# Kernel tuning notes

Hardware: AMD Instinct MI355X
Metric: run time of the kernel (lower is better)

The kernel has to match this reference:

```python
import jax, jax.numpy as jnp
import numpy as np

U = 200000   # num_users
I = 100000   # num_items
N = U + I    # total homogeneous nodes
E = 1000000  # bipartite interaction edges
D = 64       # embed_dim (== audio feature dim)
A = 20000    # num_artists
AL = 50000   # num_albums
ATTR = 8     # edge_mlp_input_dim
H = 32       # edge_mlp_hidden_dim
L = 3        # num_layers
AUDIO_SCALE = 1.0
META_SCALE = 1.0
EPS = 1e-12


def l2norm(x):
    # F.normalize(p=2, dim=-1, eps=1e-12)
    n = jnp.sqrt(jnp.sum(x * x, axis=-1, keepdims=True))
    return x / jnp.maximum(n, EPS)


def setup_inputs() -> dict:
    key = jax.random.key(0)
    ks = jax.random.split(key, 12)
    return {
        "edge_src": jax.random.randint(ks[0], (E,), 0, U, dtype=jnp.int32),
        "edge_dst": jax.random.randint(ks[1], (E,), 0, I, dtype=jnp.int32),
        "edge_attr": jax.random.normal(ks[2], (E, ATTR), dtype=jnp.float32),
        "user_w": jax.random.normal(ks[3], (U, D), dtype=jnp.float32) * 0.1,
        "artist_w": jax.random.normal(ks[4], (A, D), dtype=jnp.float32) * 0.1,
        "album_w": jax.random.normal(ks[5], (AL, D), dtype=jnp.float32) * 0.1,
        "item_audio": jax.random.normal(ks[6], (I, D), dtype=jnp.float32),
        "artist_ids": jax.random.randint(ks[7], (I,), 0, A, dtype=jnp.int32),
        "album_ids": jax.random.randint(ks[8], (I,), 0, AL, dtype=jnp.int32),
        "Wp": jax.random.normal(ks[9], (2 * D, D), dtype=jnp.float32) * (1.0 / np.sqrt(2 * D)),
        "bp": jnp.zeros((D,), dtype=jnp.float32),
        "W1": jax.random.normal(ks[10], (ATTR, H), dtype=jnp.float32) * (1.0 / np.sqrt(ATTR)),
        "b1": jnp.zeros((H,), dtype=jnp.float32),
        "W2": jax.random.normal(ks[11], (H, 1), dtype=jnp.float32) * (1.0 / np.sqrt(H)),
        "b2": jnp.zeros((1,), dtype=jnp.float32),
    }


def reference(edge_src, edge_dst, edge_attr, user_w, artist_w, album_w,
              item_audio, artist_ids, album_ids, Wp, bp, W1, b1, W2, b2):
    # --- edge-weight MLP: Linear -> ReLU -> Linear -> Sigmoid, clamp ---
    h = jax.nn.relu(edge_attr @ W1 + b1)          # [E, H]
    w = jax.nn.sigmoid(h @ W2 + b2)[:, 0]          # [E]
    w = jnp.maximum(w, 1e-6)

    # --- homogeneous graph: fwd, bwd, remaining self loops (fill=1.0) ---
    dst = edge_dst.astype(jnp.int32) + U
    loop = jnp.arange(N, dtype=jnp.int32)
    row = jnp.concatenate([edge_src, dst, loop])   # source nodes
    col = jnp.concatenate([dst, edge_src, loop])   # target nodes
    ew = jnp.concatenate([w, w, jnp.ones((N,), w.dtype)])

    # --- gcn_norm (LGConv normalize=True, add_self_loops=False inside) ---
    deg = jax.ops.segment_sum(ew, col, num_segments=N)
    dis = jnp.where(deg > 0, jax.lax.rsqrt(deg), 0.0)
    norm = dis[row] * ew * dis[col]                # [2E + N]

    # --- initial node features ---
    user = l2norm(user_w)                          # [U, D]
    meta = (artist_w[artist_ids] + album_w[album_ids]) * META_SCALE
    item_in = jnp.concatenate([item_audio * AUDIO_SCALE, meta], axis=-1)  # [I, 2D]
    item = l2norm(item_in @ Wp + bp)               # [I, D]
    x = jnp.concatenate([user, item], axis=0)      # [N, D]

    # --- L rounds of LGConv propagation, layer-sum readout ---
    acc = x
    for _ in range(L):
        x = jax.ops.segment_sum(norm[:, None] * x[row], col, num_segments=N)
        acc = acc + x
    x = l2norm(acc / (L + 1))
    return x[:U], x[U:]
```

## Files before the change

kernel.cpp:

```cpp
#include <hip/hip_runtime.h>
#include <hip/hip_bf16.h>

#define U_CNT 200000
#define I_CNT 100000
#define N_CNT 300000
#define E_CNT 1000000
#define ATTR_D 8
#define H_DIM 32
#define NB_SCAN ((N_CNT + 255) / 256)
#define IB 128
#define NB_I ((I_CNT + IB - 1) / IB)
#define NB_META (I_CNT / 16)
#define XP 130

#define BSHIFT 10
#define NBUCK 293
#define BCAP 12288
#define EPB 2048
#define NB_BIN1 ((E_CNT + EPB - 1) / EPB)


typedef unsigned short ubf;

__device__ __forceinline__ float b2f(ubf b) {
    return __uint_as_float((unsigned)b << 16);
}
__device__ __forceinline__ ubf f2b(float v) {
    unsigned u = __float_as_uint(v);
    u += 0x7fffu + ((u >> 16) & 1u);
    return (ubf)(u >> 16);
}
__device__ __forceinline__ unsigned pk2(float lo, float hi) {
    return (unsigned)f2b(lo) | ((unsigned)f2b(hi) << 16);
}
__device__ __forceinline__ float4 b4f(ushort4 u) {
    return make_float4(b2f(u.x), b2f(u.y), b2f(u.z), b2f(u.w));
}
__device__ __forceinline__ uint2 packE(int key, int partner, unsigned wb) {
    return make_uint2((unsigned)key | (((unsigned)partner & 0x1FFFu) << 19),
                     ((unsigned)partner >> 13) | (wb << 16));
}

__global__ void k_meta(const float* __restrict__ art, const float* __restrict__ alb,
                       const int* __restrict__ aid, const int* __restrict__ alid,
                       ubf* __restrict__ metabuf, int* __restrict__ gcur) {
    int t = threadIdx.x;
    if (blockIdx.x == 0) {
        for (int i = t; i < NBUCK; i += 256) gcur[i] = i * BCAP;
    }
    int lane = t & 63;
    int g = lane >> 4;
    int q = lane & 15;
    int wv = (blockIdx.x * 256 + t) >> 6;
    int it = wv * 4 + g;
    if (it >= I_CNT) return;
    int a_ = aid[it], al_ = alid[it];
    float4 va = *(const float4*)&art[(size_t)a_ * 64 + q * 4];
    float4 vb = *(const float4*)&alb[(size_t)al_ * 64 + q * 4];
    ushort4 o = make_ushort4(f2b(va.x + vb.x), f2b(va.y + vb.y),
                             f2b(va.z + vb.z), f2b(va.w + vb.w));
    *(ushort4*)&metabuf[(size_t)it * 64 + q * 4] = o;
}

__global__ void __launch_bounds__(512)
k_bin1(const int* __restrict__ src, const int* __restrict__ dst,
       const float* __restrict__ attr,
       const float* __restrict__ W1, const float* __restrict__ b1,
       const float* __restrict__ W2, const float* __restrict__ b2,
       uint2* __restrict__ ebuf, int* __restrict__ gcur) {
    __shared__ float sW1[ATTR_D * H_DIM];
    __shared__ float sb1[H_DIM];
    __shared__ float sW2[H_DIM];
    __shared__ float sb2;
    __shared__ int hist[NBUCK];
    __shared__ int basem[NBUCK];
    int t = threadIdx.x;
    if (t < 256) sW1[t] = W1[t];
    if (t < H_DIM) { sb1[t] = b1[t]; sW2[t] = W2[t]; }
    if (t == 0) sb2 = b2[0];
    for (int i = t; i < NBUCK; i += 512) hist[i] = 0;
    __syncthreads();
    int ebase = blockIdx.x * EPB;
    int sarr[4], darr[4];
    unsigned warr[4];
    #pragma unroll
    for (int k = 0; k < 4; ++k) {
        int e = ebase + k * 512 + t;
        sarr[k] = -1;
        if (e < E_CNT) {
            const float4* a4 = (const float4*)attr + (size_t)e * 2;
            float4 r0 = a4[0];
            float4 r1 = a4[1];
            float a[8] = {r0.x, r0.y, r0.z, r0.w, r1.x, r1.y, r1.z, r1.w};
            float z = sb2;
            #pragma unroll
            for (int h = 0; h < H_DIM; ++h) {
                float acc = sb1[h];
                #pragma unroll
                for (int kk = 0; kk < 8; ++kk) acc = fmaf(a[kk], sW1[kk * H_DIM + h], acc);
                acc = fmaxf(acc, 0.0f);
                z = fmaf(acc, sW2[h], z);
            }
            float w = 1.0f / (1.0f + __expf(-z));
            w = fmaxf(w, 1e-6f);
            int s = src[e], d = U_CNT + dst[e];
            sarr[k] = s; darr[k] = d; warr[k] = (unsigned)f2b(w);
            atomicAdd(&hist[s >> BSHIFT], 1);
            atomicAdd(&hist[d >> BSHIFT], 1);
        }
    }
    __syncthreads();
    for (int i = t; i < NBUCK; i += 512) {
        int h = hist[i];
        basem[i] = (h > 0) ? atomicAdd(&gcur[i], h) : 0;
    }
    __syncthreads();
    for (int i = t; i < NBUCK; i += 512) hist[i] = 0;
    __syncthreads();
    #pragma unroll
    for (int k = 0; k < 4; ++k) {
        if (sarr[k] >= 0) {
            int s = sarr[k], d = darr[k];
            unsigned wb = warr[k];
            int bs = s >> BSHIFT;
            int r = atomicAdd(&hist[bs], 1);
            ebuf[(size_t)basem[bs] + r] = packE(s, d, wb);
            int bd = d >> BSHIFT;
            r = atomicAdd(&hist[bd], 1);
            ebuf[(size_t)basem[bd] + r] = packE(d, s, wb);
        }
    }
}

__global__ void __launch_bounds__(1024)
k_bin2(const uint2* __restrict__ ebuf, const int* __restrict__ gcur,
       int* __restrict__ offs, int2* __restrict__ csr,
       float* __restrict__ dis) {
    __shared__ int ldsCnt[NBUCK];
    __shared__ int ldsH[1024];
    __shared__ int ldsC[1024];
    __shared__ int ldsT[1024];
    __shared__ float ldsW[1024];
    __shared__ int sMeta[2];
    int t = threadIdx.x;
    int b = blockIdx.x;
    if (t < NBUCK) ldsCnt[t] = gcur[t] - t * BCAP;
    ldsH[t] = 0;
    ldsC[t] = 0;
    ldsW[t] = 0.0f;
    __syncthreads();
    if (t == 0) {
        int base = 0;
        for (int i = 0; i < b; ++i) base += ldsCnt[i];
        sMeta[0] = base;
        sMeta[1] = ldsCnt[b];
    }
    __syncthreads();
    int csr_base = sMeta[0], mycount = sMeta[1];
    size_t eb = (size_t)b * BCAP;
    int first = b << BSHIFT;
    for (int i = t; i < mycount; i += 1024) {
        uint2 en = ebuf[eb + i];
        atomicAdd(&ldsH[(en.x & 0x7FFFFu) - first], 1);
    }
    __syncthreads();
    int v0 = ldsH[t];
    ldsT[t] = v0;
    __syncthreads();
    #pragma unroll
    for (int off = 1; off < 1024; off <<= 1) {
        int x = (t >= off) ? ldsT[t - off] : 0;
        __syncthreads();
        ldsT[t] += x;
        __syncthreads();
    }
    int excl = ldsT[t] - v0;
    ldsH[t] = excl;
    __syncthreads();
    int ncnt = min(1024, N_CNT - first);
    if (t < ncnt) offs[first + t] = csr_base + ldsH[t];
    if (b == NBUCK - 1 && t == 0) offs[N_CNT] = 2 * E_CNT;
    for (int i = t; i < mycount; i += 1024) {
        uint2 en = ebuf[eb + i];
        int key = (int)(en.x & 0x7FFFFu);
        int partner = (int)((en.x >> 19) | ((en.y & 0xFFFFu) << 13));
        unsigned wb = en.y >> 16;
        int li = key - first;
        int r = atomicAdd(&ldsC[li], 1);
        csr[csr_base + ldsH[li] + r] = make_int2(partner, (int)(wb << 16));
        atomicAdd(&ldsW[li], b2f((ubf)wb));
    }
    __syncthreads();
    if (t < ncnt) dis[first + t] = rsqrtf(1.0f + ldsW[t]);
}

__global__ void k_users(const float* __restrict__ user_w, const float* __restrict__ dis,
                        ubf* __restrict__ y0, float* __restrict__ acc, int use_acc) {
    int lane = threadIdx.x & 63;
    int wv = (blockIdx.x * blockDim.x + threadIdx.x) >> 6;
    int nw = (gridDim.x * blockDim.x) >> 6;
    for (int r = wv; r < U_CNT; r += nw) {
        int idx = r * 64 + lane;
        float v = user_w[idx];
        float ss = v * v;
        #pragma unroll
        for (int m = 32; m >= 1; m >>= 1) ss += __shfl_xor(ss, m, 64);
        float inv = dis[r] / fmaxf(sqrtf(ss), 1e-12f);
        float o = v * inv;
        y0[idx] = f2b(o);
        if (use_acc) acc[idx] = o;
    }
}

__global__ void __launch_bounds__(256)
k_items(const float* __restrict__ audio, const ubf* __restrict__ metabuf,
        const float* __restrict__ Wp, const float* __restrict__ bp,
        const float* __restrict__ dis,
        ubf* __restrict__ yitem, float* __restrict__ accitem, int use_acc) {
    __shared__ __align__(16) ubf sXT[128 * XP];
    __shared__ __align__(16) ubf sW[128 * 64];
    int t = threadIdx.x;
    int base = blockIdx.x * IB;
    {
        const float4* wg = (const float4*)Wp;
        #pragma unroll
        for (int r = 0; r < 8; ++r) {
            int idx = r * 256 + t;
            float4 v = wg[idx];
            ushort4 o = make_ushort4(f2b(v.x), f2b(v.y), f2b(v.z), f2b(v.w));
            *(ushort4*)&sW[idx * 4] = o;
        }
    }
    {
        const float4* g = (const float4*)audio + (size_t)base * 16;
        #pragma unroll
        for (int r = 0; r < 8; ++r) {
            int idx = r * 256 + t;
            int i = idx >> 4, fq = idx & 15;
            float4 v = make_float4(0.f, 0.f, 0.f, 0.f);
            if (base + i < I_CNT) v = g[idx];
            sXT[(4 * fq + 0) * XP + i] = f2b(v.x);
            sXT[(4 * fq + 1) * XP + i] = f2b(v.y);
            sXT[(4 * fq + 2) * XP + i] = f2b(v.z);
            sXT[(4 * fq + 3) * XP + i] = f2b(v.w);
        }
    }
    {
        const uint4* m4 = (const uint4*)(metabuf + (size_t)base * 64);
        #pragma unroll
        for (int r = 0; r < 4; ++r) {
            int idx = r * 256 + t;
            int i = idx >> 3, c = idx & 7;
            uint4 m = make_uint4(0u, 0u, 0u, 0u);
            if (base + i < I_CNT) m = m4[idx];
            ubf* dp = &sXT[(64 + 8 * c) * XP + i];
            dp[0 * XP] = (ubf)(m.x & 0xffffu); dp[1 * XP] = (ubf)(m.x >> 16);
            dp[2 * XP] = (ubf)(m.y & 0xffffu); dp[3 * XP] = (ubf)(m.y >> 16);
            dp[4 * XP] = (ubf)(m.z & 0xffffu); dp[5 * XP] = (ubf)(m.z >> 16);
            dp[6 * XP] = (ubf)(m.w & 0xffffu); dp[7 * XP] = (ubf)(m.w >> 16);
        }
    }
    __syncthreads();
    int og = t & 7;
    int igr = t >> 3;
    float c[4][8];
    {
        float bv[8];
        #pragma unroll
        for (int j = 0; j < 8; ++j) bv[j] = bp[8 * og + j];
        #pragma unroll
        for (int i = 0; i < 4; ++i)
            #pragma unroll
            for (int j = 0; j < 8; ++j) c[i][j] = bv[j];
    }
    const ubf* xcol = &sXT[4 * igr];
    const ubf* wrow = &sW[8 * og];
    #pragma unroll 2
    for (int k = 0; k < 128; ++k) {
        ushort4 xu = *(const ushort4*)&xcol[k * XP];
        uint4 wu = *(const uint4*)&wrow[k * 64];
        float x[4] = {b2f(xu.x), b2f(xu.y), b2f(xu.z), b2f(xu.w)};
        float w[8];
        w[0] = __uint_as_float(wu.x << 16); w[1] = __uint_as_float(wu.x & 0xffff0000u);
        w[2] = __uint_as_float(wu.y << 16); w[3] = __uint_as_float(wu.y & 0xffff0000u);
        w[4] = __uint_as_float(wu.z << 16); w[5] = __uint_as_float(wu.z & 0xffff0000u);
        w[6] = __uint_as_float(wu.w << 16); w[7] = __uint_as_float(wu.w & 0xffff0000u);
        #pragma unroll
        for (int i = 0; i < 4; ++i)
            #pragma unroll
            for (int j = 0; j < 8; ++j) c[i][j] = fmaf(x[i], w[j], c[i][j]);
    }
    #pragma unroll
    for (int i = 0; i < 4; ++i) {
        float ss = 0.f;
        #pragma unroll
        for (int j = 0; j < 8; ++j) ss += c[i][j] * c[i][j];
        ss += __shfl_xor(ss, 1, 64);
        ss += __shfl_xor(ss, 2, 64);
        ss += __shfl_xor(ss, 4, 64);
        int it = base + 4 * igr + i;
        if (it < I_CNT) {
            float q = dis[U_CNT + it] / fmaxf(sqrtf(ss), 1e-12f);
            uint4 o;
            o.x = pk2(c[i][0] * q, c[i][1] * q);
            o.y = pk2(c[i][2] * q, c[i][3] * q);
            o.z = pk2(c[i][4] * q, c[i][5] * q);
            o.w = pk2(c[i][6] * q, c[i][7] * q);
            *(uint4*)&yitem[(size_t)it * 64 + 8 * og] = o;
            if (use_acc) {
                float4* ap = (float4*)&accitem[(size_t)it * 64 + 8 * og];
                ap[0] = make_float4(c[i][0] * q, c[i][1] * q, c[i][2] * q, c[i][3] * q);
                ap[1] = make_float4(c[i][4] * q, c[i][5] * q, c[i][6] * q, c[i][7] * q);
            }
        }
    }
}

__device__ __forceinline__ void prop_gather(const int* offs, const int2* csr,
                                            const ubf* yin, int c, int s4,
                                            float4& a0, float4& a1,
                                            float4& a2, float4& a3) {
    int e = offs[c], end = offs[c + 1];
    for (; e + 7 < end; e += 8) {
        int2 e0 = csr[e], e1 = csr[e + 1], e2 = csr[e + 2], e3 = csr[e + 3];
        int2 e4 = csr[e + 4], e5 = csr[e + 5], e6 = csr[e + 6], e7 = csr[e + 7];
        ushort4 g0 = *(const ushort4*)&yin[(size_t)e0.x * 64 + s4];
        ushort4 g1 = *(const ushort4*)&yin[(size_t)e1.x * 64 + s4];
        ushort4 g2 = *(const ushort4*)&yin[(size_t)e2.x * 64 + s4];
        ushort4 g3 = *(const ushort4*)&yin[(size_t)e3.x * 64 + s4];
        ushort4 g4 = *(const ushort4*)&yin[(size_t)e4.x * 64 + s4];
        ushort4 g5 = *(const ushort4*)&yin[(size_t)e5.x * 64 + s4];
        ushort4 g6 = *(const ushort4*)&yin[(size_t)e6.x * 64 + s4];
        ushort4 g7 = *(const ushort4*)&yin[(size_t)e7.x * 64 + s4];
        float w0 = __int_as_float(e0.y), w1 = __int_as_float(e1.y);
        float w2 = __int_as_float(e2.y), w3 = __int_as_float(e3.y);
        float w4 = __int_as_float(e4.y), w5 = __int_as_float(e5.y);
        float w6 = __int_as_float(e6.y), w7 = __int_as_float(e7.y);
        float4 f0 = b4f(g0), f1 = b4f(g1), f2 = b4f(g2), f3 = b4f(g3);
        float4 f4 = b4f(g4), f5 = b4f(g5), f6 = b4f(g6), f7 = b4f(g7);
        a0.x = fmaf(w0, f0.x, a0.x); a0.y = fmaf(w0, f0.y, a0.y);
        a0.z = fmaf(w0, f0.z, a0.z); a0.w = fmaf(w0, f0.w, a0.w);
        a1.x = fmaf(w1, f1.x, a1.x); a1.y = fmaf(w1, f1.y, a1.y);
        a1.z = fmaf(w1, f1.z, a1.z); a1.w = fmaf(w1, f1.w, a1.w);
        a2.x = fmaf(w2, f2.x, a2.x); a2.y = fmaf(w2, f2.y, a2.y);
        a2.z = fmaf(w2, f2.z, a2.z); a2.w = fmaf(w2, f2.w, a2.w);
        a3.x = fmaf(w3, f3.x, a3.x); a3.y = fmaf(w3, f3.y, a3.y);
        a3.z = fmaf(w3, f3.z, a3.z); a3.w = fmaf(w3, f3.w, a3.w);
        a0.x = fmaf(w4, f4.x, a0.x); a0.y = fmaf(w4, f4.y, a0.y);
        a0.z = fmaf(w4, f4.z, a0.z); a0.w = fmaf(w4, f4.w, a0.w);
        a1.x = fmaf(w5, f5.x, a1.x); a1.y = fmaf(w5, f5.y, a1.y);
        a1.z = fmaf(w5, f5.z, a1.z); a1.w = fmaf(w5, f5.w, a1.w);
        a2.x = fmaf(w6, f6.x, a2.x); a2.y = fmaf(w6, f6.y, a2.y);
        a2.z = fmaf(w6, f6.z, a2.z); a2.w = fmaf(w6, f6.w, a2.w);
        a3.x = fmaf(w7, f7.x, a3.x); a3.y = fmaf(w7, f7.y, a3.y);
        a3.z = fmaf(w7, f7.z, a3.z); a3.w = fmaf(w7, f7.w, a3.w);
    }
    for (; e + 3 < end; e += 4) {
        int2 e0 = csr[e], e1 = csr[e + 1], e2 = csr[e + 2], e3 = csr[e + 3];
        ushort4 g0 = *(const ushort4*)&yin[(size_t)e0.x * 64 + s4];
        ushort4 g1 = *(const ushort4*)&yin[(size_t)e1.x * 64 + s4];
        ushort4 g2 = *(const ushort4*)&yin[(size_t)e2.x * 64 + s4];
        ushort4 g3 = *(const ushort4*)&yin[(size_t)e3.x * 64 + s4];
        float w0 = __int_as_float(e0.y), w1 = __int_as_float(e1.y);
        float w2 = __int_as_float(e2.y), w3 = __int_as_float(e3.y);
        float4 f0 = b4f(g0), f1 = b4f(g1), f2 = b4f(g2), f3 = b4f(g3);
        a0.x = fmaf(w0, f0.x, a0.x); a0.y = fmaf(w0, f0.y, a0.y);
        a0.z = fmaf(w0, f0.z, a0.z); a0.w = fmaf(w0, f0.w, a0.w);
        a1.x = fmaf(w1, f1.x, a1.x); a1.y = fmaf(w1, f1.y, a1.y);
        a1.z = fmaf(w1, f1.z, a1.z); a1.w = fmaf(w1, f1.w, a1.w);
        a2.x = fmaf(w2, f2.x, a2.x); a2.y = fmaf(w2, f2.y, a2.y);
        a2.z = fmaf(w2, f2.z, a2.z); a2.w = fmaf(w2, f2.w, a2.w);
        a3.x = fmaf(w3, f3.x, a3.x); a3.y = fmaf(w3, f3.y, a3.y);
        a3.z = fmaf(w3, f3.z, a3.z); a3.w = fmaf(w3, f3.w, a3.w);
    }
    for (; e < end; ++e) {
        int2 ee = csr[e];
        ushort4 gg = *(const ushort4*)&yin[(size_t)ee.x * 64 + s4];
        float ww = __int_as_float(ee.y);
        float4 ff = b4f(gg);
        a0.x = fmaf(ww, ff.x, a0.x); a0.y = fmaf(ww, ff.y, a0.y);
        a0.z = fmaf(ww, ff.z, a0.z); a0.w = fmaf(ww, ff.w, a0.w);
    }
}

__global__ void k_prop(const int* __restrict__ offs, const int2* __restrict__ csr,
                       const float* __restrict__ dis,
                       const ubf* __restrict__ yin, ubf* __restrict__ yout,
                       float* __restrict__ acc, int use_acc) {
    int lane = threadIdx.x & 63;
    int g = lane >> 4;
    int s4 = (lane & 15) * 4;
    int wv = (blockIdx.x * 256 + threadIdx.x) >> 6;
    int c = wv * 4 + g;
    if (c >= N_CNT) return;
    float dc = dis[c];
    float4 a0 = make_float4(0.f, 0.f, 0.f, 0.f);
    float4 a1 = a0, a2 = a0, a3 = a0;
    prop_gather(offs, csr, yin, c, s4, a0, a1, a2, a3);
    size_t idx = (size_t)c * 64 + s4;
    float4 self = b4f(*(const ushort4*)&yin[idx]);
    float dc2 = dc * dc;
    float4 r;
    r.x = dc2 * (((a0.x + a1.x) + (a2.x + a3.x)) + self.x);
    r.y = dc2 * (((a0.y + a1.y) + (a2.y + a3.y)) + self.y);
    r.z = dc2 * (((a0.z + a1.z) + (a2.z + a3.z)) + self.z);
    r.w = dc2 * (((a0.w + a1.w) + (a2.w + a3.w)) + self.w);
    *(ushort4*)&yout[idx] = make_ushort4(f2b(r.x), f2b(r.y), f2b(r.z), f2b(r.w));
    if (use_acc) {
        float4* ap = (float4*)&acc[idx];
        float4 av = *ap;
        av.x += r.x; av.y += r.y; av.z += r.z; av.w += r.w;
        *ap = av;
    }
}

__global__ void k_prop_fin(const int* __restrict__ offs, const int2* __restrict__ csr,
                           const float* __restrict__ dis,
                           const ubf* __restrict__ y0, const ubf* __restrict__ y1,
                           const ubf* __restrict__ yin, float* __restrict__ out) {
    int lane = threadIdx.x & 63;
    int g = lane >> 4;
    int s4 = (lane & 15) * 4;
    int wv = (blockIdx.x * 256 + threadIdx.x) >> 6;
    int c = wv * 4 + g;
    if (c >= N_CNT) return;
    float dc = dis[c];
    float4 a0 = make_float4(0.f, 0.f, 0.f, 0.f);
    float4 a1 = a0, a2 = a0, a3 = a0;
    prop_gather(offs, csr, yin, c, s4, a0, a1, a2, a3);
    size_t idx = (size_t)c * 64 + s4;
    float4 self = b4f(*(const ushort4*)&yin[idx]);
    float dc2 = dc * dc;
    float4 r;
    r.x = dc2 * (((a0.x + a1.x) + (a2.x + a3.x)) + self.x);
    r.y = dc2 * (((a0.y + a1.y) + (a2.y + a3.y)) + self.y);
    r.z = dc2 * (((a0.z + a1.z) + (a2.z + a3.z)) + self.z);
    r.w = dc2 * (((a0.w + a1.w) + (a2.w + a3.w)) + self.w);
    float4 v0 = b4f(*(const ushort4*)&y0[idx]);
    float4 v1 = b4f(*(const ushort4*)&y1[idx]);
    float4 v;
    v.x = (v0.x + v1.x) + (self.x + r.x);
    v.y = (v0.y + v1.y) + (self.y + r.y);
    v.z = (v0.z + v1.z) + (self.z + r.z);
    v.w = (v0.w + v1.w) + (self.w + r.w);
    float ss = v.x * v.x + v.y * v.y + v.z * v.z + v.w * v.w;
    ss += __shfl_xor(ss, 1, 64);
    ss += __shfl_xor(ss, 2, 64);
    ss += __shfl_xor(ss, 4, 64);
    ss += __shfl_xor(ss, 8, 64);
    float inv = 1.0f / fmaxf(sqrtf(ss), 1e-12f);
    *(float4*)&out[idx] = make_float4(v.x * inv, v.y * inv, v.z * inv, v.w * inv);
}

__global__ void k_final_acc(const float* __restrict__ acc, float* __restrict__ out) {
    int lane = threadIdx.x & 63;
    int c = (blockIdx.x * 256 + threadIdx.x) >> 6;
    if (c >= N_CNT) return;
    int idx = c * 64 + lane;
    float v = acc[idx];
    float ss = v * v;
    #pragma unroll
    for (int m = 32; m >= 1; m >>= 1) ss += __shfl_xor(ss, m, 64);
    out[idx] = v / fmaxf(sqrtf(ss), 1e-12f);
}

extern "C" void kernel_launch(void* const* d_in, const int* in_sizes, int n_in,
                              void* d_out, int out_size, void* d_ws, size_t ws_size,
                              hipStream_t stream) {
    const int*   edge_src   = (const int*)  d_in[0];
    const int*   edge_dst   = (const int*)  d_in[1];
    const float* edge_attr  = (const float*)d_in[2];
    const float* user_w     = (const float*)d_in[3];
    const float* artist_w   = (const float*)d_in[4];
    const float* album_w    = (const float*)d_in[5];
    const float* item_audio = (const float*)d_in[6];
    const int*   artist_ids = (const int*)  d_in[7];
    const int*   album_ids  = (const int*)  d_in[8];
    const float* Wp         = (const float*)d_in[9];
    const float* bp         = (const float*)d_in[10];
    const float* W1         = (const float*)d_in[11];
    const float* b1         = (const float*)d_in[12];
    const float* W2         = (const float*)d_in[13];
    const float* b2         = (const float*)d_in[14];

    char* p = (char*)d_ws;
    auto carve = [&](size_t bytes) -> void* {
        void* q = (void*)p;
        p += (bytes + 255) & ~(size_t)255;
        return q;
    };
    float* dis    = (float*)carve((size_t)N_CNT * 4);
    int*   offs   = (int*)  carve((size_t)(N_CNT + 1) * 4);
    int*   gcur   = (int*)  carve((size_t)NBUCK * 4);
    int2*  csr    = (int2*) carve((size_t)2 * E_CNT * 8);
    ubf*   metabuf= (ubf*)  carve((size_t)I_CNT * 64 * 2);
    const size_t YB = (size_t)N_CNT * 64 * 2;
    const size_t EBUF = (size_t)NBUCK * BCAP * 8;
    size_t used = (size_t)(p - (char*)d_ws);
    int no_acc = (ws_size >= used + 3 * YB + (size_t)4096) ? 1 : 0;
    ubf *y0, *y1, *y2;
    uint2* ebuf;
    float* acc = nullptr;
    if (no_acc) {
        y0 = (ubf*)carve(YB);
        y1 = (ubf*)carve(YB);
        y2 = (ubf*)carve(YB);
        ebuf = (uint2*)y2;
    } else {
        y0 = (ubf*)carve(YB);
        y1 = (ubf*)carve(YB);
        y2 = y0;
        acc = (float*)d_out;
        ebuf = (uint2*)carve(EBUF);
    }
    (void)in_sizes; (void)n_in; (void)out_size;

    k_meta <<<NB_META, 256, 0, stream>>>(artist_w, album_w, artist_ids,
                                         album_ids, metabuf, gcur);
    k_bin1 <<<NB_BIN1, 512, 0, stream>>>(edge_src, edge_dst, edge_attr,
                                         W1, b1, W2, b2, ebuf, gcur);
    k_bin2 <<<NBUCK, 1024, 0, stream>>>(ebuf, gcur, offs, csr, dis);
    k_users<<<1024, 256, 0, stream>>>(user_w, dis, y0, acc, no_acc ? 0 : 1);
    k_items<<<NB_I, 256, 0, stream>>>(item_audio, metabuf, Wp, bp, dis,
                                      y0 + (size_t)U_CNT * 64,
                                      no_acc ? nullptr : acc + (size_t)U_CNT * 64,
                                      no_acc ? 0 : 1);
    const int PROP_BLKS = N_CNT / 16;
    if (no_acc) {
        k_prop<<<PROP_BLKS, 256, 0, stream>>>(offs, csr, dis, y0, y1, nullptr, 0);
        k_prop<<<PROP_BLKS, 256, 0, stream>>>(offs, csr, dis, y1, y2, nullptr, 0);
        k_prop_fin<<<PROP_BLKS, 256, 0, stream>>>(offs, csr, dis, y0, y1, y2,
                                                  (float*)d_out);
    } else {
        k_prop<<<PROP_BLKS, 256, 0, stream>>>(offs, csr, dis, y0, y1, acc, 1);
        k_prop<<<PROP_BLKS, 256, 0, stream>>>(offs, csr, dis, y1, y0, acc, 1);
        k_prop<<<PROP_BLKS, 256, 0, stream>>>(offs, csr, dis, y0, y1, acc, 1);
        k_final_acc<<<N_CNT / 4, 256, 0, stream>>>(acc, (float*)d_out);
    }
}
```

Measured before the change: 513.2 us.

## Use 8 lanes per node in propagation, fuse meta into binning, wave-scan in bin2

The propagation kernels now give each node 8 lanes that each load 16 bytes (8 bf16 values), in place of 16 lanes loading 8 bytes. This halves the CSR index loads per node and widens each gather, with two accumulator sets for ILP. The meta-embedding kernel is folded into extra blocks of the binning kernel, and gcur is cleared with a memset, which removes one launch. The block scan in bin2 is replaced by a wavefront shuffle scan plus a 16-entry serial scan, which cuts the barrier count. The trade-off is lower lane parallelism per node, which may hurt latency hiding for high-degree nodes.

```diff
diff --git a/kernel.cpp b/kernel.cpp
--- a/kernel.cpp
+++ b/kernel.cpp
@@ -7,10 +7,8 @@
 #define E_CNT 1000000
 #define ATTR_D 8
 #define H_DIM 32
-#define NB_SCAN ((N_CNT + 255) / 256)
 #define IB 128
 #define NB_I ((I_CNT + IB - 1) / IB)
-#define NB_META (I_CNT / 16)
 #define XP 130
 
 #define BSHIFT 10
@@ -18,6 +16,7 @@
 #define BCAP 12288
 #define EPB 2048
 #define NB_BIN1 ((E_CNT + EPB - 1) / EPB)
+#define NB_META5 (I_CNT / 32)
 
 
 typedef unsigned short ubf;
@@ -33,33 +32,15 @@
 __device__ __forceinline__ unsigned pk2(float lo, float hi) {
     return (unsigned)f2b(lo) | ((unsigned)f2b(hi) << 16);
 }
-__device__ __forceinline__ float4 b4f(ushort4 u) {
-    return make_float4(b2f(u.x), b2f(u.y), b2f(u.z), b2f(u.w));
+__device__ __forceinline__ void unpack8(uint4 g, float f[8]) {
+    f[0] = __uint_as_float(g.x << 16); f[1] = __uint_as_float(g.x & 0xffff0000u);
+    f[2] = __uint_as_float(g.y << 16); f[3] = __uint_as_float(g.y & 0xffff0000u);
+    f[4] = __uint_as_float(g.z << 16); f[5] = __uint_as_float(g.z & 0xffff0000u);
+    f[6] = __uint_as_float(g.w << 16); f[7] = __uint_as_float(g.w & 0xffff0000u);
 }
 __device__ __forceinline__ uint2 packE(int key, int partner, unsigned wb) {
     return make_uint2((unsigned)key | (((unsigned)partner & 0x1FFFu) << 19),
                      ((unsigned)partner >> 13) | (wb << 16));
-}
-
-__global__ void k_meta(const float* __restrict__ art, const float* __restrict__ alb,
-                       const int* __restrict__ aid, const int* __restrict__ alid,
-                       ubf* __restrict__ metabuf, int* __restrict__ gcur) {
-    int t = threadIdx.x;
-    if (blockIdx.x == 0) {
-        for (int i = t; i < NBUCK; i += 256) gcur[i] = i * BCAP;
-    }
-    int lane = t & 63;
-    int g = lane >> 4;
-    int q = lane & 15;
-    int wv = (blockIdx.x * 256 + t) >> 6;
-    int it = wv * 4 + g;
-    if (it >= I_CNT) return;
-    int a_ = aid[it], al_ = alid[it];
-    float4 va = *(const float4*)&art[(size_t)a_ * 64 + q * 4];
-    float4 vb = *(const float4*)&alb[(size_t)al_ * 64 + q * 4];
-    ushort4 o = make_ushort4(f2b(va.x + vb.x), f2b(va.y + vb.y),
-                             f2b(va.z + vb.z), f2b(va.w + vb.w));
-    *(ushort4*)&metabuf[(size_t)it * 64 + q * 4] = o;
 }
 
 __global__ void __launch_bounds__(512)
@@ -67,7 +48,10 @@
        const float* __restrict__ attr,
        const float* __restrict__ W1, const float* __restrict__ b1,
        const float* __restrict__ W2, const float* __restrict__ b2,
-       uint2* __restrict__ ebuf, int* __restrict__ gcur) {
+       uint2* __restrict__ ebuf, int* __restrict__ gcur,
+       const float* __restrict__ art, const float* __restrict__ alb,
+       const int* __restrict__ aid, const int* __restrict__ alid,
+       ubf* __restrict__ metabuf) {
     __shared__ float sW1[ATTR_D * H_DIM];
     __shared__ float sb1[H_DIM];
     __shared__ float sW2[H_DIM];
@@ -75,12 +59,28 @@
     __shared__ int hist[NBUCK];
     __shared__ int basem[NBUCK];
     int t = threadIdx.x;
+    int bx = blockIdx.x;
+    if (bx >= NB_BIN1) {
+        int lane = t & 63;
+        int g = lane >> 4;
+        int q = lane & 15;
+        int wv = ((bx - NB_BIN1) * 512 + t) >> 6;
+        int it = wv * 4 + g;
+        if (it >= I_CNT) return;
+        int a_ = aid[it], al_ = alid[it];
+        float4 va = *(const float4*)&art[(size_t)a_ * 64 + q * 4];
+        float4 vb = *(const float4*)&alb[(size_t)al_ * 64 + q * 4];
+        ushort4 o = make_ushort4(f2b(va.x + vb.x), f2b(va.y + vb.y),
+                                 f2b(va.z + vb.z), f2b(va.w + vb.w));
+        *(ushort4*)&metabuf[(size_t)it * 64 + q * 4] = o;
+        return;
+    }
     if (t < 256) sW1[t] = W1[t];
     if (t < H_DIM) { sb1[t] = b1[t]; sW2[t] = W2[t]; }
     if (t == 0) sb2 = b2[0];
     for (int i = t; i < NBUCK; i += 512) hist[i] = 0;
     __syncthreads();
-    int ebase = blockIdx.x * EPB;
+    int ebase = bx * EPB;
     int sarr[4], darr[4];
     unsigned warr[4];
     #pragma unroll
@@ -112,7 +112,7 @@
     __syncthreads();
     for (int i = t; i < NBUCK; i += 512) {
         int h = hist[i];
-        basem[i] = (h > 0) ? atomicAdd(&gcur[i], h) : 0;
+        basem[i] = (h > 0) ? (i * BCAP + atomicAdd(&gcur[i], h)) : 0;
     }
     __syncthreads();
     for (int i = t; i < NBUCK; i += 512) hist[i] = 0;
@@ -139,12 +139,12 @@
     __shared__ int ldsCnt[NBUCK];
     __shared__ int ldsH[1024];
     __shared__ int ldsC[1024];
-    __shared__ int ldsT[1024];
     __shared__ float ldsW[1024];
+    __shared__ int ldsT[16];
     __shared__ int sMeta[2];
     int t = threadIdx.x;
     int b = blockIdx.x;
-    if (t < NBUCK) ldsCnt[t] = gcur[t] - t * BCAP;
+    if (t < NBUCK) ldsCnt[t] = gcur[t];
     ldsH[t] = 0;
     ldsC[t] = 0;
     ldsW[t] = 0.0f;
@@ -165,16 +165,22 @@
     }
     __syncthreads();
     int v0 = ldsH[t];
-    ldsT[t] = v0;
-    __syncthreads();
-    #pragma unroll
-    for (int off = 1; off < 1024; off <<= 1) {
-        int x = (t >= off) ? ldsT[t - off] : 0;
-        __syncthreads();
-        ldsT[t] += x;
-        __syncthreads();
-    }
-    int excl = ldsT[t] - v0;
+    int incl = v0;
+    #pragma unroll
+    for (int off = 1; off < 64; off <<= 1) {
+        int x = __shfl_up(incl, off, 64);
+        if ((t & 63) >= off) incl += x;
+    }
+    int w = t >> 6;
+    if ((t & 63) == 63) ldsT[w] = incl;
+    __syncthreads();
+    if (t == 0) {
+        int run = 0;
+        #pragma unroll
+        for (int i = 0; i < 16; ++i) { int x = ldsT[i]; ldsT[i] = run; run += x; }
+    }
+    __syncthreads();
+    int excl = ldsT[w] + incl - v0;
     ldsH[t] = excl;
     __syncthreads();
     int ncnt = min(1024, N_CNT - first);
@@ -281,10 +287,7 @@
         uint4 wu = *(const uint4*)&wrow[k * 64];
         float x[4] = {b2f(xu.x), b2f(xu.y), b2f(xu.z), b2f(xu.w)};
         float w[8];
-        w[0] = __uint_as_float(wu.x << 16); w[1] = __uint_as_float(wu.x & 0xffff0000u);
-        w[2] = __uint_as_float(wu.y << 16); w[3] = __uint_as_float(wu.y & 0xffff0000u);
-        w[4] = __uint_as_float(wu.z << 16); w[5] = __uint_as_float(wu.z & 0xffff0000u);
-        w[6] = __uint_as_float(wu.w << 16); w[7] = __uint_as_float(wu.w & 0xffff0000u);
+        unpack8(wu, w);
         #pragma unroll
         for (int i = 0; i < 4; ++i)
             #pragma unroll
@@ -316,71 +319,88 @@
     }
 }
 
-__device__ __forceinline__ void prop_gather(const int* offs, const int2* csr,
-                                            const ubf* yin, int c, int s4,
-                                            float4& a0, float4& a1,
-                                            float4& a2, float4& a3) {
+__device__ __forceinline__ void prop_gather(const int* __restrict__ offs,
+                                            const int2* __restrict__ csr,
+                                            const ubf* __restrict__ yin,
+                                            int c, int s8, float* acc) {
     int e = offs[c], end = offs[c + 1];
+    float bcc[8];
+    #pragma unroll
+    for (int i = 0; i < 8; ++i) bcc[i] = 0.f;
     for (; e + 7 < end; e += 8) {
-        int2 e0 = csr[e], e1 = csr[e + 1], e2 = csr[e + 2], e3 = csr[e + 3];
-        int2 e4 = csr[e + 4], e5 = csr[e + 5], e6 = csr[e + 6], e7 = csr[e + 7];
-        ushort4 g0 = *(const ushort4*)&yin[(size_t)e0.x * 64 + s4];
-        ushort4 g1 = *(const ushort4*)&yin[(size_t)e1.x * 64 + s4];
-        ushort4 g2 = *(const ushort4*)&yin[(size_t)e2.x * 64 + s4];
-        ushort4 g3 = *(const ushort4*)&yin[(size_t)e3.x * 64 + s4];
-        ushort4 g4 = *(const ushort4*)&yin[(size_t)e4.x * 64 + s4];
-        ushort4 g5 = *(const ushort4*)&yin[(size_t)e5.x * 64 + s4];
-        ushort4 g6 = *(const ushort4*)&yin[(size_t)e6.x * 64 + s4];
-        ushort4 g7 = *(const ushort4*)&yin[(size_t)e7.x * 64 + s4];
-        float w0 = __int_as_float(e0.y), w1 = __int_as_float(e1.y);
-        float w2 = __int_as_float(e2.y), w3 = __int_as_float(e3.y);
-        float w4 = __int_as_float(e4.y), w5 = __int_as_float(e5.y);
-        float w6 = __int_as_float(e6.y), w7 = __int_as_float(e7.y);
-        float4 f0 = b4f(g0), f1 = b4f(g1), f2 = b4f(g2), f3 = b4f(g3);
-        float4 f4 = b4f(g4), f5 = b4f(g5), f6 = b4f(g6), f7 = b4f(g7);
-        a0.x = fmaf(w0, f0.x, a0.x); a0.y = fmaf(w0, f0.y, a0.y);
-        a0.z = fmaf(w0, f0.z, a0.z); a0.w = fmaf(w0, f0.w, a0.w);
-        a1.x = fmaf(w1, f1.x, a1.x); a1.y = fmaf(w1, f1.y, a1.y);
-        a1.z = fmaf(w1, f1.z, a1.z); a1.w = fmaf(w1, f1.w, a1.w);
-        a2.x = fmaf(w2, f2.x, a2.x); a2.y = fmaf(w2, f2.y, a2.y);
-        a2.z = fmaf(w2, f2.z, a2.z); a2.w = fmaf(w2, f2.w, a2.w);
-        a3.x = fmaf(w3, f3.x, a3.x); a3.y = fmaf(w3, f3.y, a3.y);
-        a3.z = fmaf(w3, f3.z, a3.z); a3.w = fmaf(w3, f3.w, a3.w);
-        a0.x = fmaf(w4, f4.x, a0.x); a0.y = fmaf(w4, f4.y, a0.y);
-        a0.z = fmaf(w4, f4.z, a0.z); a0.w = fmaf(w4, f4.w, a0.w);
-        a1.x = fmaf(w5, f5.x, a1.x); a1.y = fmaf(w5, f5.y, a1.y);
-        a1.z = fmaf(w5, f5.z, a1.z); a1.w = fmaf(w5, f5.w, a1.w);
-        a2.x = fmaf(w6, f6.x, a2.x); a2.y = fmaf(w6, f6.y, a2.y);
-        a2.z = fmaf(w6, f6.z, a2.z); a2.w = fmaf(w6, f6.w, a2.w);
-        a3.x = fmaf(w7, f7.x, a3.x); a3.y = fmaf(w7, f7.y, a3.y);
-        a3.z = fmaf(w7, f7.z, a3.z); a3.w = fmaf(w7, f7.w, a3.w);
+        int2 c0 = csr[e], c1 = csr[e + 1], c2 = csr[e + 2], c3 = csr[e + 3];
+        int2 c4 = csr[e + 4], c5 = csr[e + 5], c6 = csr[e + 6], c7 = csr[e + 7];
+        uint4 g0 = *(const uint4*)&yin[(size_t)c0.x * 64 + s8];
+        uint4 g1 = *(const uint4*)&yin[(size_t)c1.x * 64 + s8];
+        uint4 g2 = *(const uint4*)&yin[(size_t)c2.x * 64 + s8];
+        uint4 g3 = *(const uint4*)&yin[(size_t)c3.x * 64 + s8];
+        uint4 g4 = *(const uint4*)&yin[(size_t)c4.x * 64 + s8];
+        uint4 g5 = *(const uint4*)&yin[(size_t)c5.x * 64 + s8];
+        uint4 g6 = *(const uint4*)&yin[(size_t)c6.x * 64 + s8];
+        uint4 g7 = *(const uint4*)&yin[(size_t)c7.x * 64 + s8];
+        float f[8];
+        float w0 = __int_as_float(c0.y), w1 = __int_as_float(c1.y);
+        float w2 = __int_as_float(c2.y), w3 = __int_as_float(c3.y);
+        float w4 = __int_as_float(c4.y), w5 = __int_as_float(c5.y);
+        float w6 = __int_as_float(c6.y), w7 = __int_as_float(c7.y);
+        unpack8(g0, f);
+        #pragma unroll
+        for (int i = 0; i < 8; ++i) acc[i] = fmaf(w0, f[i], acc[i]);
+        unpack8(g1, f);
+        #pragma unroll
+        for (int i = 0; i < 8; ++i) bcc[i] = fmaf(w1, f[i], bcc[i]);
+        unpack8(g2, f);
+        #pragma unroll
+        for (int i = 0; i < 8; ++i) acc[i] = fmaf(w2, f[i], acc[i]);
+        unpack8(g3, f);
+        #pragma unroll
+        for (int i = 0; i < 8; ++i) bcc[i] = fmaf(w3, f[i], bcc[i]);
+        unpack8(g4, f);
+        #pragma unroll
+        for (int i = 0; i < 8; ++i) acc[i] = fmaf(w4, f[i], acc[i]);
+        unpack8(g5, f);
+        #pragma unroll
+        for (int i = 0; i < 8; ++i) bcc[i] = fmaf(w5, f[i], bcc[i]);
+        unpack8(g6, f);
+        #pragma unroll
+        for (int i = 0; i < 8; ++i) acc[i] = fmaf(w6, f[i], acc[i]);
+        unpack8(g7, f);
+        #pragma unroll
+        for (int i = 0; i < 8; ++i) bcc[i] = fmaf(w7, f[i], bcc[i]);
     }
     for (; e + 3 < end; e += 4) {
-        int2 e0 = csr[e], e1 = csr[e + 1], e2 = csr[e + 2], e3 = csr[e + 3];
-        ushort4 g0 = *(const ushort4*)&yin[(size_t)e0.x * 64 + s4];
-        ushort4 g1 = *(const ushort4*)&yin[(size_t)e1.x * 64 + s4];
-        ushort4 g2 = *(const ushort4*)&yin[(size_t)e2.x * 64 + s4];
-        ushort4 g3 = *(const ushort4*)&yin[(size_t)e3.x * 64 + s4];
-        float w0 = __int_as_float(e0.y), w1 = __int_as_float(e1.y);
-        float w2 = __int_as_float(e2.y), w3 = __int_as_float(e3.y);
-        float4 f0 = b4f(g0), f1 = b4f(g1), f2 = b4f(g2), f3 = b4f(g3);
-        a0.x = fmaf(w0, f0.x, a0.x); a0.y = fmaf(w0, f0.y, a0.y);
-        a0.z = fmaf(w0, f0.z, a0.z); a0.w = fmaf(w0, f0.w, a0.w);
-        a1.x = fmaf(w1, f1.x, a1.x); a1.y = fmaf(w1, f1.y, a1.y);
-        a1.z = fmaf(w1, f1.z, a1.z); a1.w = fmaf(w1, f1.w, a1.w);
-        a2.x = fmaf(w2, f2.x, a2.x); a2.y = fmaf(w2, f2.y, a2.y);
-        a2.z = fmaf(w2, f2.z, a2.z); a2.w = fmaf(w2, f2.w, a2.w);
-        a3.x = fmaf(w3, f3.x, a3.x); a3.y = fmaf(w3, f3.y, a3.y);
-        a3.z = fmaf(w3, f3.z, a3.z); a3.w = fmaf(w3, f3.w, a3.w);
+        int2 c0 = csr[e], c1 = csr[e + 1], c2 = csr[e + 2], c3 = csr[e + 3];
+        uint4 g0 = *(const uint4*)&yin[(size_t)c0.x * 64 + s8];
+        uint4 g1 = *(const uint4*)&yin[(size_t)c1.x * 64 + s8];
+        uint4 g2 = *(const uint4*)&yin[(size_t)c2.x * 64 + s8];
+        uint4 g3 = *(const uint4*)&yin[(size_t)c3.x * 64 + s8];
+        float f[8];
+        float w0 = __int_as_float(c0.y), w1 = __int_as_float(c1.y);
+        float w2 = __int_as_float(c2.y), w3 = __int_as_float(c3.y);
+        unpack8(g0, f);
+        #pragma unroll
+        for (int i = 0; i < 8; ++i) acc[i] = fmaf(w0, f[i], acc[i]);
+        unpack8(g1, f);
+        #pragma unroll
+        for (int i = 0; i < 8; ++i) bcc[i] = fmaf(w1, f[i], bcc[i]);
+        unpack8(g2, f);
+        #pragma unroll
+        for (int i = 0; i < 8; ++i) acc[i] = fmaf(w2, f[i], acc[i]);
+        unpack8(g3, f);
+        #pragma unroll
+        for (int i = 0; i < 8; ++i) bcc[i] = fmaf(w3, f[i], bcc[i]);
     }
     for (; e < end; ++e) {
-        int2 ee = csr[e];
-        ushort4 gg = *(const ushort4*)&yin[(size_t)ee.x * 64 + s4];
-        float ww = __int_as_float(ee.y);
-        float4 ff = b4f(gg);
-        a0.x = fmaf(ww, ff.x, a0.x); a0.y = fmaf(ww, ff.y, a0.y);
-        a0.z = fmaf(ww, ff.z, a0.z); a0.w = fmaf(ww, ff.w, a0.w);
-    }
+        int2 cc = csr[e];
+        uint4 gg = *(const uint4*)&yin[(size_t)cc.x * 64 + s8];
+        float f[8];
+        float ww = __int_as_float(cc.y);
+        unpack8(gg, f);
+        #pragma unroll
+        for (int i = 0; i < 8; ++i) acc[i] = fmaf(ww, f[i], acc[i]);
+    }
+    #pragma unroll
+    for (int i = 0; i < 8; ++i) acc[i] += bcc[i];
 }
 
 __global__ void k_prop(const int* __restrict__ offs, const int2* __restrict__ csr,
@@ -388,29 +408,34 @@
                        const ubf* __restrict__ yin, ubf* __restrict__ yout,
                        float* __restrict__ acc, int use_acc) {
     int lane = threadIdx.x & 63;
-    int g = lane >> 4;
-    int s4 = (lane & 15) * 4;
+    int g = lane >> 3;
+    int s8 = (lane & 7) * 8;
     int wv = (blockIdx.x * 256 + threadIdx.x) >> 6;
-    int c = wv * 4 + g;
+    int c = wv * 8 + g;
     if (c >= N_CNT) return;
     float dc = dis[c];
-    float4 a0 = make_float4(0.f, 0.f, 0.f, 0.f);
-    float4 a1 = a0, a2 = a0, a3 = a0;
-    prop_gather(offs, csr, yin, c, s4, a0, a1, a2, a3);
-    size_t idx = (size_t)c * 64 + s4;
-    float4 self = b4f(*(const ushort4*)&yin[idx]);
+    float a[8];
+    #pragma unroll
+    for (int i = 0; i < 8; ++i) a[i] = 0.f;
+    prop_gather(offs, csr, yin, c, s8, a);
+    size_t idx = (size_t)c * 64 + s8;
+    uint4 sv = *(const uint4*)&yin[idx];
+    float sf[8];
+    unpack8(sv, sf);
     float dc2 = dc * dc;
-    float4 r;
-    r.x = dc2 * (((a0.x + a1.x) + (a2.x + a3.x)) + self.x);
-    r.y = dc2 * (((a0.y + a1.y) + (a2.y + a3.y)) + self.y);
-    r.z = dc2 * (((a0.z + a1.z) + (a2.z + a3.z)) + self.z);
-    r.w = dc2 * (((a0.w + a1.w) + (a2.w + a3.w)) + self.w);
-    *(ushort4*)&yout[idx] = make_ushort4(f2b(r.x), f2b(r.y), f2b(r.z), f2b(r.w));
+    float r[8];
+    #pragma unroll
+    for (int i = 0; i < 8; ++i) r[i] = dc2 * (a[i] + sf[i]);
+    uint4 o;
+    o.x = pk2(r[0], r[1]); o.y = pk2(r[2], r[3]);
+    o.z = pk2(r[4], r[5]); o.w = pk2(r[6], r[7]);
+    *(uint4*)&yout[idx] = o;
     if (use_acc) {
         float4* ap = (float4*)&acc[idx];
-        float4 av = *ap;
-        av.x += r.x; av.y += r.y; av.z += r.z; av.w += r.w;
-        *ap = av;
+        float4 a0 = ap[0], a1 = ap[1];
+        a0.x += r[0]; a0.y += r[1]; a0.z += r[2]; a0.w += r[3];
+        a1.x += r[4]; a1.y += r[5]; a1.z += r[6]; a1.w += r[7];
+        ap[0] = a0; ap[1] = a1;
     }
 }
 
@@ -419,37 +444,40 @@
                            const ubf* __restrict__ y0, const ubf* __restrict__ y1,
                            const ubf* __restrict__ yin, float* __restrict__ out) {
     int lane = threadIdx.x & 63;
-    int g = lane >> 4;
-    int s4 = (lane & 15) * 4;
+    int g = lane >> 3;
+    int s8 = (lane & 7) * 8;
     int wv = (blockIdx.x * 256 + threadIdx.x) >> 6;
-    int c = wv * 4 + g;
+    int c = wv * 8 + g;
     if (c >= N_CNT) return;
     float dc = dis[c];
-    float4 a0 = make_float4(0.f, 0.f, 0.f, 0.f);
-    float4 a1 = a0, a2 = a0, a3 = a0;
-    prop_gather(offs, csr, yin, c, s4, a0, a1, a2, a3);
-    size_t idx = (size_t)c * 64 + s4;
-    float4 self = b4f(*(const ushort4*)&yin[idx]);
+    float a[8];
+    #pragma unroll
+    for (int i = 0; i < 8; ++i) a[i] = 0.f;
+    prop_gather(offs, csr, yin, c, s8, a);
+    size_t idx = (size_t)c * 64 + s8;
+    uint4 sv = *(const uint4*)&yin[idx];
+    uint4 v0u = *(const uint4*)&y0[idx];
+    uint4 v1u = *(const uint4*)&y1[idx];
+    float sf[8], f0[8], f1[8];
+    unpack8(sv, sf);
+    unpack8(v0u, f0);
+    unpack8(v1u, f1);
     float dc2 = dc * dc;
-    float4 r;
-    r.x = dc2 * (((a0.x + a1.x) + (a2.x + a3.x)) + self.x);
-    r.y = dc2 * (((a0.y + a1.y) + (a2.y + a3.y)) + self.y);
-    r.z = dc2 * (((a0.z + a1.z) + (a2.z + a3.z)) + self.z);
-    r.w = dc2 * (((a0.w + a1.w) + (a2.w + a3.w)) + self.w);
-    float4 v0 = b4f(*(const ushort4*)&y0[idx]);
-    float4 v1 = b4f(*(const ushort4*)&y1[idx]);
-    float4 v;
-    v.x = (v0.x + v1.x) + (self.x + r.x);
-    v.y = (v0.y + v1.y) + (self.y + r.y);
-    v.z = (v0.z + v1.z) + (self.z + r.z);
-    v.w = (v0.w + v1.w) + (self.w + r.w);
-    float ss = v.x * v.x + v.y * v.y + v.z * v.z + v.w * v.w;
+    float v[8];
+    float ss = 0.f;
+    #pragma unroll
+    for (int i = 0; i < 8; ++i) {
+        float r = dc2 * (a[i] + sf[i]);
+        v[i] = (f0[i] + f1[i]) + (sf[i] + r);
+        ss = fmaf(v[i], v[i], ss);
+    }
     ss += __shfl_xor(ss, 1, 64);
     ss += __shfl_xor(ss, 2, 64);
     ss += __shfl_xor(ss, 4, 64);
-    ss += __shfl_xor(ss, 8, 64);
     float inv = 1.0f / fmaxf(sqrtf(ss), 1e-12f);
-    *(float4*)&out[idx] = make_float4(v.x * inv, v.y * inv, v.z * inv, v.w * inv);
+    float4* op = (float4*)&out[idx];
+    op[0] = make_float4(v[0] * inv, v[1] * inv, v[2] * inv, v[3] * inv);
+    op[1] = make_float4(v[4] * inv, v[5] * inv, v[6] * inv, v[7] * inv);
 }
 
 __global__ void k_final_acc(const float* __restrict__ acc, float* __restrict__ out) {
@@ -515,17 +543,17 @@
     }
     (void)in_sizes; (void)n_in; (void)out_size;
 
-    k_meta <<<NB_META, 256, 0, stream>>>(artist_w, album_w, artist_ids,
-                                         album_ids, metabuf, gcur);
-    k_bin1 <<<NB_BIN1, 512, 0, stream>>>(edge_src, edge_dst, edge_attr,
-                                         W1, b1, W2, b2, ebuf, gcur);
+    hipMemsetAsync(gcur, 0, (size_t)NBUCK * 4, stream);
+    k_bin1 <<<NB_BIN1 + NB_META5, 512, 0, stream>>>(
+        edge_src, edge_dst, edge_attr, W1, b1, W2, b2, ebuf, gcur,
+        artist_w, album_w, artist_ids, album_ids, metabuf);
     k_bin2 <<<NBUCK, 1024, 0, stream>>>(ebuf, gcur, offs, csr, dis);
     k_users<<<1024, 256, 0, stream>>>(user_w, dis, y0, acc, no_acc ? 0 : 1);
     k_items<<<NB_I, 256, 0, stream>>>(item_audio, metabuf, Wp, bp, dis,
                                       y0 + (size_t)U_CNT * 64,
                                       no_acc ? nullptr : acc + (size_t)U_CNT * 64,
                                       no_acc ? 0 : 1);
-    const int PROP_BLKS = N_CNT / 16;
+    const int PROP_BLKS = N_CNT / 32;
     if (no_acc) {
         k_prop<<<PROP_BLKS, 256, 0, stream>>>(offs, csr, dis, y0, y1, nullptr, 0);
         k_prop<<<PROP_BLKS, 256, 0, stream>>>(offs, csr, dis, y1, y2, nullptr, 0);
```

Measured after the change: 499.4 us. 1.03x faster.
